# Kernel tuning notes

Hardware: AMD Instinct MI355X
Metric: run time of the kernel (lower is better)

## Reference

```python
import jax, jax.numpy as jnp
import numpy as np

NBINS = 256

def _equalize_flat(flat):
    # flat: [N, P] int32 pixel values in [0,255], N = B*C channels, P = H*W pixels
    N, P = flat.shape
    hist = jax.vmap(lambda v: jnp.bincount(v, length=NBINS))(flat)  # [N, 256]
    bins = jnp.arange(NBINS, dtype=jnp.int32)
    # last nonzero bin value per channel (PIL: drop last nonzero entry from the step sum)
    last_idx = jnp.max(jnp.where(hist != 0, bins[None, :], -1), axis=1)  # [N]
    last_val = jnp.take_along_axis(hist, last_idx[:, None], axis=1)[:, 0]  # [N]
    step = (P - last_val) // 255  # [N] integer floor div
    safe_step = jnp.maximum(step, 1)
    cs = jnp.cumsum(hist, axis=1)  # [N, 256]
    lut = (cs + (step // 2)[:, None]) // safe_step[:, None]
    # pad left with 0, drop last, clamp to [0,255]
    lut = jnp.concatenate([jnp.zeros((N, 1), lut.dtype), lut[:, :-1]], axis=1)
    lut = jnp.clip(lut, 0, 255)
    eq = jnp.take_along_axis(lut, flat, axis=1)  # [N, P]
    # channels with step==0 pass through unchanged
    return jnp.where((step == 0)[:, None], flat, eq)


def setup_inputs() -> dict:
    key = jax.random.key(0)
    img = jax.random.randint(key, (64, 3, 512, 512), 0, 256).astype(jnp.float32)
    return {"img": img}


def reference(img) -> jnp.ndarray:
    B, C, H, W = img.shape
    flat = img.astype(jnp.int32).reshape(B * C, H * W)
    out = _equalize_flat(flat)
    return out.reshape(B, C, H, W).astype(img.dtype)
```

## Files before the change

### kernel.cpp

```cpp
#include <hip/hip_runtime.h>


#define NBINS 256
#define NCOPY 16
#define BPC_H 16
#define BPC_A 4
#define CHUNK_H 16384
#define CHUNK_A 65536
#define NVEC_H (CHUNK_H / 4)
#define NVEC_A (CHUNK_A / 4)

typedef float vfloat4 __attribute__((ext_vector_type(4)));

__global__ __launch_bounds__(256, 8) void eq_hist_pack_kernel(
    const float* __restrict__ in, unsigned int* __restrict__ pack,
    unsigned int* __restrict__ phist) {
    __shared__ unsigned int lh[NBINS * NCOPY];
    const int t = threadIdx.x;
    const int copy = t & (NCOPY - 1);

    for (int i = t; i < NBINS * NCOPY; i += 256) lh[i] = 0u;
    __syncthreads();

    const size_t basev = (size_t)blockIdx.x * NVEC_H;
    const float4* vin = (const float4*)in + basev;
    unsigned int* pout = pack + basev;

    #pragma unroll 4
    for (int i = t; i < NVEC_H; i += 256) {
        float4 v = vin[i];
        int ix = min(max((int)v.x, 0), 255);
        int iy = min(max((int)v.y, 0), 255);
        int iz = min(max((int)v.z, 0), 255);
        int iw = min(max((int)v.w, 0), 255);
        atomicAdd(&lh[ix * NCOPY + copy], 1u);
        atomicAdd(&lh[iy * NCOPY + copy], 1u);
        atomicAdd(&lh[iz * NCOPY + copy], 1u);
        atomicAdd(&lh[iw * NCOPY + copy], 1u);
        pout[i] = (unsigned)ix | ((unsigned)iy << 8) |
                  ((unsigned)iz << 16) | ((unsigned)iw << 24);
    }
    __syncthreads();

    unsigned int hsum = 0;
    #pragma unroll
    for (int c = 0; c < NCOPY; ++c)
        hsum += lh[t * NCOPY + ((t + c) & (NCOPY - 1))];
    phist[(size_t)blockIdx.x * NBINS + t] = hsum;
}

__global__ __launch_bounds__(256) void eq_lut_apply_kernel(
    const unsigned int* __restrict__ pack, const unsigned int* __restrict__ phist,
    float* __restrict__ out, int P) {
    __shared__ float slut[NBINS * 32];
    __shared__ unsigned int s[NBINS];
    __shared__ int sidx[NBINS];
    const int t = threadIdx.x;
    const int copy = t & 31;
    const int chan = blockIdx.x >> 2;

    unsigned int h = 0;
    const unsigned int* pb = phist + (size_t)chan * BPC_H * NBINS;
    #pragma unroll
    for (int b = 0; b < BPC_H; ++b) h += pb[b * NBINS + t];
    s[t] = h;
    sidx[t] = (h != 0u) ? t : -1;
    __syncthreads();

    for (int off = 128; off > 0; off >>= 1) {
        if (t < off) sidx[t] = max(sidx[t], sidx[t + off]);
        __syncthreads();
    }
    const int last_idx = sidx[0];
    const int last_val = (int)s[last_idx];
    const int step = (P - last_val) / 255;

    for (int off = 1; off < NBINS; off <<= 1) {
        unsigned int v = (t >= off) ? s[t - off] : 0u;
        __syncthreads();
        s[t] += v;
        __syncthreads();
    }

    float lv;
    if (step == 0) {
        lv = (float)t;
    } else {
        int csp = (t == 0) ? 0 : (int)s[t - 1];
        lv = (float)min(max((csp + (step >> 1)) / step, 0), 255);
    }
    #pragma unroll
    for (int c = 0; c < 32; ++c)
        slut[t * 32 + ((t + c) & 31)] = lv;
    __syncthreads();

    const size_t basev = (size_t)blockIdx.x * NVEC_A;
    const unsigned int* pin = pack + basev;
    vfloat4* vout = (vfloat4*)out + basev;

    #pragma unroll 4
    for (int i = t; i < NVEC_A; i += 256) {
        unsigned int p = pin[i];
        vfloat4 r;
        r.x = slut[(p & 255u) * 32 + copy];
        r.y = slut[((p >> 8) & 255u) * 32 + copy];
        r.z = slut[((p >> 16) & 255u) * 32 + copy];
        r.w = slut[(p >> 24) * 32 + copy];
        __builtin_nontemporal_store(r, &vout[i]);
    }
}

extern "C" void kernel_launch(void* const* d_in, const int* in_sizes, int n_in,
                              void* d_out, int out_size, void* d_ws, size_t ws_size,
                              hipStream_t stream) {
    const float* img = (const float*)d_in[0];
    float* out = (float*)d_out;

    const int P = 512 * 512;
    const int total = in_sizes[0];
    const int N = total / P;

    unsigned int* pack  = (unsigned int*)d_ws;
    unsigned int* phist = (unsigned int*)((char*)d_ws + (size_t)total);

    eq_hist_pack_kernel<<<N * BPC_H, 256, 0, stream>>>(img, pack, phist);
    eq_lut_apply_kernel<<<N * BPC_A, 256, 0, stream>>>(pack, phist, out, P);
}
```

Baseline: 353.0 us.

## Retune histogram and apply kernels: wider sub-histograms, smaller LUT copies, uint2 loads

The histogram kernel now uses 4 blocks per channel instead of 16, each processing 64K pixels, with 32 per-lane sub-histogram copies instead of 16 and no occupancy hint. The apply kernel uses 8 blocks per channel with only 8 LUT copies, freeing LDS for higher occupancy (launch bound 6), and each thread reads a uint2 of packed indices and writes two float4s. The aim is less atomic contention, less LUT setup and more memory parallelism. The cost is fewer histogram blocks overall and more LDS bank conflicts on the smaller LUT.

```diff
diff --git a/kernel.cpp b/kernel.cpp
--- a/kernel.cpp
+++ b/kernel.cpp
@@ -2,24 +2,22 @@
 
 
 #define NBINS 256
-#define NCOPY 16
-#define BPC_H 16
-#define BPC_A 4
-#define CHUNK_H 16384
-#define CHUNK_A 65536
-#define NVEC_H (CHUNK_H / 4)
-#define NVEC_A (CHUNK_A / 4)
+#define BPC_H 4
+#define BPC_A 8
+#define NVEC_H 16384
+#define NVEC2_A 4096
+#define NCOPY_A 8
 
 typedef float vfloat4 __attribute__((ext_vector_type(4)));
 
-__global__ __launch_bounds__(256, 8) void eq_hist_pack_kernel(
+__global__ __launch_bounds__(256) void eq_hist_pack_kernel(
     const float* __restrict__ in, unsigned int* __restrict__ pack,
     unsigned int* __restrict__ phist) {
-    __shared__ unsigned int lh[NBINS * NCOPY];
+    __shared__ unsigned int lh[NBINS * 32];
     const int t = threadIdx.x;
-    const int copy = t & (NCOPY - 1);
+    const int copy = t & 31;
 
-    for (int i = t; i < NBINS * NCOPY; i += 256) lh[i] = 0u;
+    for (int i = t; i < NBINS * 32; i += 256) lh[i] = 0u;
     __syncthreads();
 
     const size_t basev = (size_t)blockIdx.x * NVEC_H;
@@ -33,10 +31,10 @@
         int iy = min(max((int)v.y, 0), 255);
         int iz = min(max((int)v.z, 0), 255);
         int iw = min(max((int)v.w, 0), 255);
-        atomicAdd(&lh[ix * NCOPY + copy], 1u);
-        atomicAdd(&lh[iy * NCOPY + copy], 1u);
-        atomicAdd(&lh[iz * NCOPY + copy], 1u);
-        atomicAdd(&lh[iw * NCOPY + copy], 1u);
+        atomicAdd(&lh[ix * 32 + copy], 1u);
+        atomicAdd(&lh[iy * 32 + copy], 1u);
+        atomicAdd(&lh[iz * 32 + copy], 1u);
+        atomicAdd(&lh[iw * 32 + copy], 1u);
         pout[i] = (unsigned)ix | ((unsigned)iy << 8) |
                   ((unsigned)iz << 16) | ((unsigned)iw << 24);
     }
@@ -44,20 +42,19 @@
 
     unsigned int hsum = 0;
     #pragma unroll
-    for (int c = 0; c < NCOPY; ++c)
-        hsum += lh[t * NCOPY + ((t + c) & (NCOPY - 1))];
+    for (int c = 0; c < 32; ++c) hsum += lh[t * 32 + ((t + c) & 31)];
     phist[(size_t)blockIdx.x * NBINS + t] = hsum;
 }
 
-__global__ __launch_bounds__(256) void eq_lut_apply_kernel(
+__global__ __launch_bounds__(256, 6) void eq_lut_apply_kernel(
     const unsigned int* __restrict__ pack, const unsigned int* __restrict__ phist,
     float* __restrict__ out, int P) {
-    __shared__ float slut[NBINS * 32];
+    __shared__ float slut[NBINS * NCOPY_A];
     __shared__ unsigned int s[NBINS];
     __shared__ int sidx[NBINS];
     const int t = threadIdx.x;
-    const int copy = t & 31;
-    const int chan = blockIdx.x >> 2;
+    const int copy = t & (NCOPY_A - 1);
+    const int chan = blockIdx.x >> 3;
 
     unsigned int h = 0;
     const unsigned int* pb = phist + (size_t)chan * BPC_H * NBINS;
@@ -90,23 +87,28 @@
         lv = (float)min(max((csp + (step >> 1)) / step, 0), 255);
     }
     #pragma unroll
-    for (int c = 0; c < 32; ++c)
-        slut[t * 32 + ((t + c) & 31)] = lv;
+    for (int c = 0; c < NCOPY_A; ++c)
+        slut[t * NCOPY_A + ((t + c) & (NCOPY_A - 1))] = lv;
     __syncthreads();
 
-    const size_t basev = (size_t)blockIdx.x * NVEC_A;
-    const unsigned int* pin = pack + basev;
-    vfloat4* vout = (vfloat4*)out + basev;
+    const size_t base2 = (size_t)blockIdx.x * NVEC2_A;
+    const uint2* pin = (const uint2*)pack + base2;
+    vfloat4* vout = (vfloat4*)out + base2 * 2;
 
     #pragma unroll 4
-    for (int i = t; i < NVEC_A; i += 256) {
-        unsigned int p = pin[i];
-        vfloat4 r;
-        r.x = slut[(p & 255u) * 32 + copy];
-        r.y = slut[((p >> 8) & 255u) * 32 + copy];
-        r.z = slut[((p >> 16) & 255u) * 32 + copy];
-        r.w = slut[(p >> 24) * 32 + copy];
-        __builtin_nontemporal_store(r, &vout[i]);
+    for (int i = t; i < NVEC2_A; i += 256) {
+        uint2 p = pin[i];
+        vfloat4 r0, r1;
+        r0.x = slut[(p.x & 255u) * NCOPY_A + copy];
+        r0.y = slut[((p.x >> 8) & 255u) * NCOPY_A + copy];
+        r0.z = slut[((p.x >> 16) & 255u) * NCOPY_A + copy];
+        r0.w = slut[(p.x >> 24) * NCOPY_A + copy];
+        r1.x = slut[(p.y & 255u) * NCOPY_A + copy];
+        r1.y = slut[((p.y >> 8) & 255u) * NCOPY_A + copy];
+        r1.z = slut[((p.y >> 16) & 255u) * NCOPY_A + copy];
+        r1.w = slut[(p.y >> 24) * NCOPY_A + copy];
+        __builtin_nontemporal_store(r0, &vout[2 * i]);
+        __builtin_nontemporal_store(r1, &vout[2 * i + 1]);
     }
 }
 
```

Result: slower. 408.0 us (+15.6%).
